# Performance work log

Hardware: AMD Instinct MI355X
Metric: run time of the kernel (lower is better)

## Reference

```python
import jax, jax.numpy as jnp
import numpy as np

B, T, H, W, C = 2, 8, 64, 64, 192
WIN = (4, 8, 8)
SHIFT = (2, 4, 4)
HEADS = 6
HID = 4 * C
N = WIN[0] * WIN[1] * WIN[2]  # 256 tokens per window
CPB_HID = 512


def window_partition(x, win):
    b, t, h, w, c = x.shape
    x = x.reshape(b, t // win[0], win[0], h // win[1], win[1], w // win[2], win[2], c)
    x = x.transpose(0, 1, 3, 5, 2, 4, 6, 7)
    return x.reshape(-1, win[0] * win[1] * win[2], c)


def window_reverse(wins, win, b, t, h, w):
    x = wins.reshape(b, t // win[0], h // win[1], w // win[2], win[0], win[1], win[2], -1)
    x = x.transpose(0, 1, 4, 2, 5, 3, 6, 7)
    return x.reshape(b, t, h, w, -1)


def _rel_coords_table():
    axes = [np.arange(-(WIN[i] - 1), WIN[i], dtype=np.float32) for i in range(3)]
    tbl = np.stack(np.meshgrid(*axes, indexing='ij'), axis=-1)  # (2wt-1,2wh-1,2ww-1,3)
    for i in range(3):
        tbl[..., i] /= WIN[i] - 1
    tbl *= 8.0
    tbl = np.sign(tbl) * np.log2(np.abs(tbl) + 1.0) / np.log2(8.0)
    return tbl.reshape(-1, 3)


def _rel_pos_index():
    coords = np.stack(np.meshgrid(np.arange(WIN[0]), np.arange(WIN[1]), np.arange(WIN[2]), indexing='ij'))
    cf = coords.reshape(3, -1)
    rel = (cf[:, :, None] - cf[:, None, :]).transpose(1, 2, 0)
    rel[..., 0] += WIN[0] - 1
    rel[..., 1] += WIN[1] - 1
    rel[..., 2] += WIN[2] - 1
    rel[..., 0] *= (2 * WIN[1] - 1) * (2 * WIN[2] - 1)
    rel[..., 1] *= 2 * WIN[2] - 1
    return rel.sum(-1)  # (N, N) int


def _attn_mask():
    img = np.zeros((1, T, H, W, 1), dtype=np.float32)
    cnt = 0
    for d in (slice(-WIN[0]), slice(-WIN[0], -SHIFT[0]), slice(-SHIFT[0], None)):
        for h in (slice(-WIN[1]), slice(-WIN[1], -SHIFT[1]), slice(-SHIFT[1], None)):
            for w in (slice(-WIN[2]), slice(-WIN[2], -SHIFT[2]), slice(-SHIFT[2], None)):
                img[:, d, h, w, :] = cnt
                cnt += 1
    mw = window_partition(img, WIN).squeeze(-1)  # (nW, N)
    am = mw[:, None, :] - mw[:, :, None]
    return np.where(am != 0, -100.0, 0.0).astype(np.float32)


REL_TABLE = jnp.asarray(_rel_coords_table())      # (M, 3)
RPI = jnp.asarray(_rel_pos_index().reshape(-1))   # (N*N,)
MASK = jnp.asarray(_attn_mask())                  # (nW, N, N)


def _ln(x, g, b):
    m = x.mean(-1, keepdims=True)
    v = x.var(-1, keepdims=True)
    return (x - m) / jnp.sqrt(v + 1e-5) * g + b


def setup_inputs() -> dict:
    key = jax.random.key(0)
    ks = jax.random.split(key, 16)
    s = lambda fan: 1.0 / np.sqrt(fan)
    return {
        'x': jax.random.normal(ks[0], (B, T, H, W, C), jnp.float32),
        'qkv_w': jax.random.normal(ks[1], (3 * C, C), jnp.float32) * s(C),
        'qkv_b': jnp.zeros((3 * C,), jnp.float32),
        'proj_w': jax.random.normal(ks[2], (C, C), jnp.float32) * s(C),
        'proj_b': jnp.zeros((C,), jnp.float32),
        'cpb_w1': jax.random.normal(ks[3], (CPB_HID, 3), jnp.float32) * s(3),
        'cpb_b1': jnp.zeros((CPB_HID,), jnp.float32),
        'cpb_w2': jax.random.normal(ks[4], (HEADS, CPB_HID), jnp.float32) * s(CPB_HID),
        'logit_scale': jnp.log(10.0 * jnp.ones((HEADS, 1, 1), jnp.float32)),
        'norm1_g': jnp.ones((C,), jnp.float32),
        'norm1_b': jnp.zeros((C,), jnp.float32),
        'norm2_g': jnp.ones((C,), jnp.float32),
        'norm2_b': jnp.zeros((C,), jnp.float32),
        'fc1_w': jax.random.normal(ks[5], (HID, C), jnp.float32) * s(C),
        'fc1_b': jnp.zeros((HID,), jnp.float32),
        'fc2_w': jax.random.normal(ks[6], (C, HID), jnp.float32) * s(HID),
        'fc2_b': jnp.zeros((C,), jnp.float32),
    }


def reference(x, qkv_w, qkv_b, proj_w, proj_b, cpb_w1, cpb_b1, cpb_w2,
              logit_scale, norm1_g, norm1_b, norm2_g, norm2_b,
              fc1_w, fc1_b, fc2_w, fc2_b):
    shortcut = x
    # cyclic shift
    xs = jnp.roll(x, shift=(-SHIFT[0], -SHIFT[1], -SHIFT[2]), axis=(1, 2, 3))
    xw = window_partition(xs, WIN)  # (B*nW, N, C)
    B_ = xw.shape[0]
    d = C // HEADS
    qkv = (xw @ qkv_w.T + qkv_b).reshape(B_, N, 3, HEADS, d).transpose(2, 0, 3, 1, 4)
    q, k, v = qkv[0], qkv[1], qkv[2]  # (B_, h, N, d)
    # cosine attention (F.normalize eps=1e-12)
    qn = q / jnp.maximum(jnp.linalg.norm(q, axis=-1, keepdims=True), 1e-12)
    kn = k / jnp.maximum(jnp.linalg.norm(k, axis=-1, keepdims=True), 1e-12)
    attn = jnp.einsum('bhnd,bhmd->bhnm', qn, kn)
    scale = jnp.exp(jnp.minimum(logit_scale, jnp.log(100.0)))  # clamp at log(1/0.01)
    attn = attn * scale
    # continuous relative position bias
    tbl = jax.nn.relu(REL_TABLE @ cpb_w1.T + cpb_b1) @ cpb_w2.T  # (M, heads)
    bias = tbl[RPI].reshape(N, N, HEADS).transpose(2, 0, 1)      # (h, N, N)
    attn = attn + 16.0 * jax.nn.sigmoid(bias)[None]
    # shift mask
    nW = MASK.shape[0]
    attn = attn.reshape(B_ // nW, nW, HEADS, N, N) + MASK[None, :, None]
    attn = jax.nn.softmax(attn.reshape(B_, HEADS, N, N), axis=-1)
    out = jnp.einsum('bhnm,bhmd->bhnd', attn, v)
    out = out.transpose(0, 2, 1, 3).reshape(B_, N, C)
    out = out @ proj_w.T + proj_b
    xr = window_reverse(out, WIN, B, T, H, W)
    xr = jnp.roll(xr, shift=SHIFT, axis=(1, 2, 3))
    # SwinV2 res-post-norm residual
    x = shortcut + _ln(xr, norm1_g, norm1_b)
    h1 = jax.nn.gelu(x @ fc1_w.T + fc1_b, approximate=False)
    x = x + _ln(h1 @ fc2_w.T + fc2_b, norm2_g, norm2_b)
    return x
```

## Files before the change

### kernel.cpp

```cpp
#include <hip/hip_runtime.h>
#include <math.h>


typedef short short8 __attribute__((ext_vector_type(8)));
typedef short short4v __attribute__((ext_vector_type(4)));
typedef float f32x4 __attribute__((ext_vector_type(4)));

__device__ __forceinline__ short f2bf(float f) {
    union { float f; unsigned u; } v; v.f = f;
    unsigned r = v.u + 0x7FFF + ((v.u >> 16) & 1);
    return (short)(r >> 16);
}

__device__ __forceinline__ float gelu_fast(float x) {
    float s = x * x;
    float t = fmaf(0.044715f, s, 1.0f);
    float y = -1.5957691216057308f * x * t;
    return x * __builtin_amdgcn_rcpf(1.0f + __expf(y));
}

__global__ __launch_bounds__(64) void pack_w_k(const float* __restrict__ w,
                                               short* __restrict__ dst, int K) {
    int lane = threadIdx.x;
    int ktn = K >> 5;
    int nt = blockIdx.x / ktn, kt = blockIdx.x % ktn;
    int r = lane & 15, q = lane >> 4;
    const float* src = w + (size_t)(nt * 16 + r) * K + kt * 32 + q * 8;
    short8 v;
#pragma unroll
    for (int j = 0; j < 8; j++) v[j] = f2bf(src[j]);
    ((short8*)dst)[(size_t)blockIdx.x * 64 + lane] = v;
}

__global__ __launch_bounds__(64) void cpb_table_k(const float* __restrict__ w1,
                                                  const float* __restrict__ b1,
                                                  const float* __restrict__ w2,
                                                  float* __restrict__ tbl6) {
    int m = blockIdx.x;
    int lane = threadIdx.x;
    int it = m / 225;
    int ih = (m / 15) % 15;
    int iw = m % 15;
    float r0 = (float)(it - 3) * (8.0f / 3.0f);
    float r1 = (float)(ih - 7) * (8.0f / 7.0f);
    float r2 = (float)(iw - 7) * (8.0f / 7.0f);
    float c0 = (r0 < 0.f ? -1.f : 1.f) * log2f(fabsf(r0) + 1.0f) * (1.0f / 3.0f);
    float c1 = (r1 < 0.f ? -1.f : 1.f) * log2f(fabsf(r1) + 1.0f) * (1.0f / 3.0f);
    float c2 = (r2 < 0.f ? -1.f : 1.f) * log2f(fabsf(r2) + 1.0f) * (1.0f / 3.0f);
    float hv[8];
#pragma unroll
    for (int j = 0; j < 8; j++) {
        int t = lane * 8 + j;
        hv[j] = fmaxf(0.0f, c0 * w1[3 * t] + c1 * w1[3 * t + 1] + c2 * w1[3 * t + 2] + b1[t]);
    }
#pragma unroll
    for (int head = 0; head < 6; head++) {
        float s = 0.f;
#pragma unroll
        for (int j = 0; j < 8; j++) s += hv[j] * w2[head * 512 + lane * 8 + j];
        s += __shfl_xor(s, 1);
        s += __shfl_xor(s, 2);
        s += __shfl_xor(s, 4);
        s += __shfl_xor(s, 8);
        s += __shfl_xor(s, 16);
        s += __shfl_xor(s, 32);
        if (lane == 0) tbl6[m * 6 + head] = s;
    }
}

__global__ __launch_bounds__(256) void bias_k(const float* __restrict__ tbl6,
                                              float* __restrict__ biasT) {
    int idx = blockIdx.x * 256 + threadIdx.x;
    int h = idx >> 16;
    int rem = idx & 65535;
    int jj = rem >> 8, ii = rem & 255;
    int dt = (ii >> 6) - (jj >> 6) + 3;
    int dh = ((ii >> 3) & 7) - ((jj >> 3) & 7) + 7;
    int dw = (ii & 7) - (jj & 7) + 7;
    int rel = dt * 225 + dh * 15 + dw;
    float v = tbl6[rel * 6 + h];
    biasT[idx] = 16.0f / (1.0f + expf(-v));
}

#define ZSTR 388
__global__ __launch_bounds__(256) void qkv_mfma_k(const float* __restrict__ x,
                                                  const short* __restrict__ wqp,
                                                  const float* __restrict__ qkv_b,
                                                  short* __restrict__ qbf,
                                                  short* __restrict__ kbf,
                                                  short* __restrict__ vtb) {
    __shared__ float Z[32 * ZSTR];
    int tid = threadIdx.x, lane = tid & 63, w = tid >> 6;
    int r = lane & 15, q = lane >> 4;
    int b_ = blockIdx.x >> 3, n0 = (blockIdx.x & 7) << 5;
    int b = b_ >> 7, win = b_ & 127;
    int wt = win >> 6, wh = (win >> 3) & 7, ww = win & 7;

    short8 af[2][6];
#pragma unroll
    for (int m = 0; m < 2; m++) {
        int n = n0 + m * 16 + r;
        int t0 = ((wt * 4 + (n >> 6)) + 2) & 7;
        int h0 = ((wh * 8 + ((n >> 3) & 7)) + 4) & 63;
        int w0 = ((ww * 8 + (n & 7)) + 4) & 63;
        const float* src = x + ((size_t)((b * 8 + t0) * 64 + h0) * 64 + w0) * 192 + q * 8;
#pragma unroll
        for (int kt = 0; kt < 6; kt++) {
            float4 x0 = *(const float4*)(src + kt * 32);
            float4 x1 = *(const float4*)(src + kt * 32 + 4);
            short8 v;
            v[0] = f2bf(x0.x); v[1] = f2bf(x0.y); v[2] = f2bf(x0.z); v[3] = f2bf(x0.w);
            v[4] = f2bf(x1.x); v[5] = f2bf(x1.y); v[6] = f2bf(x1.z); v[7] = f2bf(x1.w);
            af[m][kt] = v;
        }
    }

    for (int ntl = 0; ntl < 9; ntl++) {
        int nt = w * 9 + ntl;
        float bias = qkv_b[nt * 16 + r];
        short8 bfr[6];
#pragma unroll
        for (int kt = 0; kt < 6; kt++)
            bfr[kt] = ((const short8*)wqp)[(size_t)(nt * 6 + kt) * 64 + lane];
        f32x4 a0 = {bias, bias, bias, bias};
        f32x4 a1 = {bias, bias, bias, bias};
#pragma unroll
        for (int kt = 0; kt < 6; kt++) {
            a0 = __builtin_amdgcn_mfma_f32_16x16x32_bf16(af[0][kt], bfr[kt], a0, 0, 0, 0);
            a1 = __builtin_amdgcn_mfma_f32_16x16x32_bf16(af[1][kt], bfr[kt], a1, 0, 0, 0);
        }
        int col = nt * 16 + r;
        if (nt < 24) {
#pragma unroll
            for (int reg = 0; reg < 4; reg++) {
                Z[(q * 4 + reg) * ZSTR + col] = a0[reg];
                Z[(16 + q * 4 + reg) * ZSTR + col] = a1[reg];
            }
        } else {
            int ch = col - 384;
            int hh = ch >> 5, dd = ch & 31;
            short* vb = vtb + ((size_t)(b_ * 6 + hh) * 32 + dd) * 256 + n0;
            short4v p0, p1;
#pragma unroll
            for (int reg = 0; reg < 4; reg++) { p0[reg] = f2bf(a0[reg]); p1[reg] = f2bf(a1[reg]); }
            *(short4v*)(vb + q * 4) = p0;
            *(short4v*)(vb + 16 + q * 4) = p1;
        }
    }
    __syncthreads();
    for (int rw = tid; rw < 384; rw += 256) {
        int token = rw / 12, rr = rw - token * 12;
        int isq = rr < 6 ? 1 : 0;
        int h = isq ? rr : rr - 6;
        const float* rp = &Z[token * ZSTR + rr * 32];
        float ss = 0.f;
#pragma unroll
        for (int d4 = 0; d4 < 8; d4++) {
            f32x4 v4 = *(const f32x4*)(rp + d4 * 4);
            ss += v4[0] * v4[0] + v4[1] * v4[1] + v4[2] * v4[2] + v4[3] * v4[3];
        }
        float inv = 1.0f / fmaxf(sqrtf(ss), 1e-12f);
        short* dst = (isq ? qbf : kbf) + ((size_t)(b_ * 6 + h) * 256 + n0 + token) * 32;
#pragma unroll
        for (int d8 = 0; d8 < 4; d8++) {
            f32x4 a4 = *(const f32x4*)(rp + d8 * 8);
            f32x4 b4 = *(const f32x4*)(rp + d8 * 8 + 4);
            short8 v;
            v[0] = f2bf(a4[0] * inv); v[1] = f2bf(a4[1] * inv);
            v[2] = f2bf(a4[2] * inv); v[3] = f2bf(a4[3] * inv);
            v[4] = f2bf(b4[0] * inv); v[5] = f2bf(b4[1] * inv);
            v[6] = f2bf(b4[2] * inv); v[7] = f2bf(b4[3] * inv);
            *(short8*)(dst + d8 * 8) = v;
        }
    }
}

#define KSTR 40
#define VSTR 264
#define PSTR 40
__global__ __launch_bounds__(256) void attn_mfma_k(const short* __restrict__ qbf,
                                                   const short* __restrict__ kbf,
                                                   const short* __restrict__ vtb,
                                                   const float* __restrict__ biasT,
                                                   const float* __restrict__ logit_scale,
                                                   short* __restrict__ att) {
    __shared__ short Ks[256 * KSTR];
    __shared__ short Vs[32 * VSTR];
    __shared__ short Ps[4][16 * PSTR];
    int tid = threadIdx.x, lane = tid & 63, w = tid >> 6;
    int r = lane & 15, q = lane >> 4;
    int b_ = blockIdx.x / 6, h = blockIdx.x % 6;
    size_t base = (size_t)(b_ * 6 + h) * 8192;

    const short8* kg = (const short8*)(kbf + base);
    const short8* vg = (const short8*)(vtb + base);
    for (int i = tid; i < 1024; i += 256) {
        short8 kv = kg[i];
        *(short8*)&Ks[(i >> 2) * KSTR + (i & 3) * 8] = kv;
        short8 vv = vg[i];
        *(short8*)&Vs[(i >> 5) * VSTR + (i & 31) * 8] = vv;
    }

    short8 qf[4];
#pragma unroll
    for (int mt = 0; mt < 4; mt++)
        qf[mt] = *(const short8*)(qbf + base + (size_t)(w * 64 + mt * 16 + r) * 32 + q * 8);

    float scale = __expf(fminf(logit_scale[h], 4.6051702f));
    float M = scale + 16.0f;
    int win = b_ & 127;
    int wt4 = (win >> 6) * 4, wh8 = ((win >> 3) & 7) * 8, ww8 = (win & 7) * 8;
    auto region = [&](int n) {
        int ts = wt4 + (n >> 6), hs = wh8 + ((n >> 3) & 7), wsv = ww8 + (n & 7);
        int rt = ts < 4 ? 0 : (ts < 6 ? 1 : 2);
        int rh = hs < 56 ? 0 : (hs < 60 ? 1 : 2);
        int rw = wsv < 56 ? 0 : (wsv < 60 ? 1 : 2);
        return rt * 9 + rh * 3 + rw;
    };
    int rowreg[4][4];
#pragma unroll
    for (int mt = 0; mt < 4; mt++)
#pragma unroll
        for (int reg = 0; reg < 4; reg++)
            rowreg[mt][reg] = region(w * 64 + mt * 16 + q * 4 + reg);

    f32x4 O[4][2];
    float lp[4][4];
#pragma unroll
    for (int mt = 0; mt < 4; mt++) {
        O[mt][0] = (f32x4){0.f, 0.f, 0.f, 0.f};
        O[mt][1] = (f32x4){0.f, 0.f, 0.f, 0.f};
#pragma unroll
        for (int reg = 0; reg < 4; reg++) lp[mt][reg] = 0.f;
    }
    __syncthreads();

    const float* bh = biasT + ((size_t)h << 16);
    for (int s = 0; s < 8; s++) {
        short8 kf0 = *(const short8*)&Ks[(s * 32 + r) * KSTR + q * 8];
        short8 kf1 = *(const short8*)&Ks[(s * 32 + 16 + r) * KSTR + q * 8];
        short8 vf0 = *(const short8*)&Vs[r * VSTR + s * 32 + q * 8];
        short8 vf1 = *(const short8*)&Vs[(16 + r) * VSTR + s * 32 + q * 8];
        int cr0 = region(s * 32 + r);
        int cr1 = region(s * 32 + 16 + r);
#pragma unroll
        for (int mt = 0; mt < 4; mt++) {
            f32x4 s0 = {0.f, 0.f, 0.f, 0.f};
            f32x4 s1 = {0.f, 0.f, 0.f, 0.f};
            s0 = __builtin_amdgcn_mfma_f32_16x16x32_bf16(qf[mt], kf0, s0, 0, 0, 0);
            s1 = __builtin_amdgcn_mfma_f32_16x16x32_bf16(qf[mt], kf1, s1, 0, 0, 0);
            int qcol = w * 64 + mt * 16 + q * 4;
            float4 b0 = *(const float4*)(bh + (size_t)(s * 32 + r) * 256 + qcol);
            float4 b1 = *(const float4*)(bh + (size_t)(s * 32 + 16 + r) * 256 + qcol);
#pragma unroll
            for (int reg = 0; reg < 4; reg++) {
                float bb0 = (reg == 0 ? b0.x : reg == 1 ? b0.y : reg == 2 ? b0.z : b0.w);
                float bb1 = (reg == 0 ? b1.x : reg == 1 ? b1.y : reg == 2 ? b1.z : b1.w);
                float v0 = s0[reg] * scale + bb0 + (cr0 == rowreg[mt][reg] ? 0.f : -100.f) - M;
                float v1 = s1[reg] * scale + bb1 + (cr1 == rowreg[mt][reg] ? 0.f : -100.f) - M;
                float p0 = __expf(v0);
                float p1 = __expf(v1);
                lp[mt][reg] += p0 + p1;
                Ps[w][(q * 4 + reg) * PSTR + r] = f2bf(p0);
                Ps[w][(q * 4 + reg) * PSTR + 16 + r] = f2bf(p1);
            }
            short8 pa = *(const short8*)&Ps[w][r * PSTR + q * 8];
            O[mt][0] = __builtin_amdgcn_mfma_f32_16x16x32_bf16(vf0, pa, O[mt][0], 0, 0, 0);
            O[mt][1] = __builtin_amdgcn_mfma_f32_16x16x32_bf16(vf1, pa, O[mt][1], 0, 0, 0);
        }
    }

#pragma unroll
    for (int mt = 0; mt < 4; mt++)
#pragma unroll
        for (int reg = 0; reg < 4; reg++) {
            float v = lp[mt][reg];
            v += __shfl_xor(v, 1);
            v += __shfl_xor(v, 2);
            v += __shfl_xor(v, 4);
            v += __shfl_xor(v, 8);
            lp[mt][reg] = 1.0f / v;
        }
#pragma unroll
    for (int mt = 0; mt < 4; mt++) {
        int srcl = (r >> 2) << 4;
        float t0 = __shfl(lp[mt][0], srcl);
        float t1 = __shfl(lp[mt][1], srcl);
        float t2 = __shfl(lp[mt][2], srcl);
        float t3 = __shfl(lp[mt][3], srcl);
        int rm = r & 3;
        float linv = rm == 0 ? t0 : (rm == 1 ? t1 : (rm == 2 ? t2 : t3));
        int query = w * 64 + mt * 16 + r;
        short* dst = att + ((size_t)b_ * 256 + query) * 192 + h * 32 + q * 4;
#pragma unroll
        for (int nt = 0; nt < 2; nt++) {
            short4v pv;
#pragma unroll
            for (int reg = 0; reg < 4; reg++) pv[reg] = f2bf(O[mt][nt][reg] * linv);
            *(short4v*)(dst + nt * 16) = pv;
        }
    }
}

__global__ __launch_bounds__(256) void proj_mfma_k(const short* __restrict__ att,
                                                   const short* __restrict__ wpp,
                                                   const float* __restrict__ proj_b,
                                                   const float* __restrict__ x,
                                                   const float* __restrict__ g1,
                                                   const float* __restrict__ b1n,
                                                   float* __restrict__ out,
                                                   short* __restrict__ xmb) {
    __shared__ float Z[32 * 196];
    __shared__ float ps[32][8];
    __shared__ float pss[32][8];
    __shared__ float mean_s[32], inv_s[32];
    int tid = threadIdx.x, lane = tid & 63, w = tid >> 6;
    int r = lane & 15, q = lane >> 4;
    int b_ = blockIdx.x >> 3, n0 = (blockIdx.x & 7) << 5;

    short8 af[2][6];
#pragma unroll
    for (int m = 0; m < 2; m++) {
        const short* src = att + ((size_t)b_ * 256 + n0 + m * 16 + r) * 192 + q * 8;
#pragma unroll
        for (int kt = 0; kt < 6; kt++)
            af[m][kt] = *(const short8*)(src + kt * 32);
    }
    for (int ntl = 0; ntl < 3; ntl++) {
        int nt = w * 3 + ntl;
        f32x4 binit = *(const f32x4*)(proj_b + nt * 16 + q * 4);
        short8 bfr[6];
#pragma unroll
        for (int kt = 0; kt < 6; kt++)
            bfr[kt] = ((const short8*)wpp)[(size_t)(nt * 6 + kt) * 64 + lane];
        f32x4 a0 = binit, a1 = binit;
#pragma unroll
        for (int kt = 0; kt < 6; kt++) {
            a0 = __builtin_amdgcn_mfma_f32_16x16x32_bf16(bfr[kt], af[0][kt], a0, 0, 0, 0);
            a1 = __builtin_amdgcn_mfma_f32_16x16x32_bf16(bfr[kt], af[1][kt], a1, 0, 0, 0);
        }
        *(f32x4*)&Z[(r) * 196 + nt * 16 + q * 4] = a0;
        *(f32x4*)&Z[(16 + r) * 196 + nt * 16 + q * 4] = a1;
    }
    __syncthreads();
    {
        int token = tid >> 3, part = tid & 7;
        float s = 0.f, ss = 0.f;
        const float* zr = &Z[token * 196 + part * 24];
#pragma unroll
        for (int c = 0; c < 24; c++) { float v = zr[c]; s += v; ss += v * v; }
        ps[token][part] = s; pss[token][part] = ss;
    }
    __syncthreads();
    if (tid < 32) {
        float s = 0.f, ss = 0.f;
#pragma unroll
        for (int p = 0; p < 8; p++) { s += ps[tid][p]; ss += pss[tid][p]; }
        float mean = s * (1.0f / 192.0f);
        float var = ss * (1.0f / 192.0f) - mean * mean;
        mean_s[tid] = mean;
        inv_s[tid] = 1.0f / sqrtf(var + 1e-5f);
    }
    __syncthreads();
    int b = b_ >> 7, win = b_ & 127;
    int wt = win >> 6, wh = (win >> 3) & 7, ww = win & 7;
#pragma unroll
    for (int k = 0; k < 6; k++) {
        int idx = k * 256 + tid;
        int token = idx / 48;
        int c4 = (idx - token * 48) * 4;
        int n = n0 + token;
        int t0 = ((wt * 4 + (n >> 6)) + 2) & 7;
        int h0 = ((wh * 8 + ((n >> 3) & 7)) + 4) & 63;
        int w0 = ((ww * 8 + (n & 7)) + 4) & 63;
        size_t gb = ((size_t)((b * 8 + t0) * 64 + h0) * 64 + w0) * 192 + c4;
        float mean = mean_s[token], inv = inv_s[token];
        f32x4 zv = *(const f32x4*)&Z[token * 196 + c4];
        f32x4 gv = *(const f32x4*)(g1 + c4);
        f32x4 bv = *(const f32x4*)(b1n + c4);
        f32x4 xv = *(const f32x4*)(x + gb);
        f32x4 o;
        short4v xm;
#pragma unroll
        for (int j = 0; j < 4; j++) {
            o[j] = xv[j] + (zv[j] - mean) * inv * gv[j] + bv[j];
            xm[j] = f2bf(o[j]);
        }
        *(f32x4*)(out + gb) = o;
        *(short4v*)(xmb + gb) = xm;
    }
}

#define XSTR 200
#define H2STR 264
__global__ __launch_bounds__(512, 4) void mlp_mfma_k(const short* __restrict__ xmb,
                                                     const short* __restrict__ w1p,
                                                     const short* __restrict__ w2p,
                                                     const float* __restrict__ fc1_b,
                                                     const float* __restrict__ fc2_b,
                                                     const float* __restrict__ g2,
                                                     const float* __restrict__ b2,
                                                     float* __restrict__ out) {
    __shared__ short Xs[64 * XSTR];
    __shared__ short Hs[64 * H2STR];
    __shared__ float ps[64][4], pss[64][4];
    __shared__ float mean_s[64], inv_s[64];
    int tid = threadIdx.x;
    int lane = tid & 63, w = tid >> 6;
    int r = lane & 15, q = lane >> 4;
    size_t tok0 = (size_t)blockIdx.x * 64;

    for (int i = tid; i < 1536; i += 512) {
        int token = i / 24, ch8 = (i - token * 24) * 8;
        short8 v = *(const short8*)(xmb + (tok0 + token) * 192 + ch8);
        *(short8*)&Xs[token * XSTR + ch8] = v;
    }
    __syncthreads();

    int mg = w >> 2;
    int ng = w & 3;
    f32x4 acc2[6];
#pragma unroll
    for (int i = 0; i < 6; i++) acc2[i] = (f32x4){0.f, 0.f, 0.f, 0.f};

    for (int c = 0; c < 3; c++) {
        {
            int ntg0 = c * 16 + 2 * w;
            f32x4 a[2][4];
#pragma unroll
            for (int ntl = 0; ntl < 2; ntl++) {
                f32x4 binit = *(const f32x4*)(fc1_b + (ntg0 + ntl) * 16 + q * 4);
#pragma unroll
                for (int m = 0; m < 4; m++) a[ntl][m] = binit;
            }
#pragma unroll
            for (int kt = 0; kt < 6; kt++) {
                short8 w0 = ((const short8*)w1p)[(size_t)((ntg0) * 6 + kt) * 64 + lane];
                short8 w1f = ((const short8*)w1p)[(size_t)((ntg0 + 1) * 6 + kt) * 64 + lane];
                short8 xb[4];
#pragma unroll
                for (int m = 0; m < 4; m++)
                    xb[m] = *(const short8*)&Xs[(m * 16 + r) * XSTR + kt * 32 + q * 8];
#pragma unroll
                for (int m = 0; m < 4; m++) {
                    a[0][m] = __builtin_amdgcn_mfma_f32_16x16x32_bf16(w0, xb[m], a[0][m], 0, 0, 0);
                    a[1][m] = __builtin_amdgcn_mfma_f32_16x16x32_bf16(w1f, xb[m], a[1][m], 0, 0, 0);
                }
            }
#pragma unroll
            for (int ntl = 0; ntl < 2; ntl++) {
                int hcol = (2 * w + ntl) * 16 + q * 4;
#pragma unroll
                for (int m = 0; m < 4; m++) {
                    short4v p;
#pragma unroll
                    for (int reg = 0; reg < 4; reg++) p[reg] = f2bf(gelu_fast(a[ntl][m][reg]));
                    *(short4v*)&Hs[(m * 16 + r) * H2STR + hcol] = p;
                }
            }
        }
        __syncthreads();

#pragma unroll
        for (int kk = 0; kk < 8; kk++) {
            short8 hb0 = *(const short8*)&Hs[((mg * 2) * 16 + r) * H2STR + kk * 32 + q * 8];
            short8 hb1 = *(const short8*)&Hs[((mg * 2 + 1) * 16 + r) * H2STR + kk * 32 + q * 8];
            int kkg = c * 8 + kk;
#pragma unroll
            for (int n = 0; n < 3; n++) {
                int ntz = ng * 3 + n;
                short8 wf = ((const short8*)w2p)[(size_t)(ntz * 24 + kkg) * 64 + lane];
                acc2[n * 2 + 0] = __builtin_amdgcn_mfma_f32_16x16x32_bf16(wf, hb0, acc2[n * 2 + 0], 0, 0, 0);
                acc2[n * 2 + 1] = __builtin_amdgcn_mfma_f32_16x16x32_bf16(wf, hb1, acc2[n * 2 + 1], 0, 0, 0);
            }
        }
        __syncthreads();
    }

    float s0 = 0.f, ss0 = 0.f, s1 = 0.f, ss1 = 0.f;
#pragma unroll
    for (int n = 0; n < 3; n++) {
        f32x4 b4 = *(const f32x4*)(fc2_b + (ng * 3 + n) * 16 + q * 4);
        f32x4 z0 = acc2[n * 2 + 0] + b4;
        f32x4 z1 = acc2[n * 2 + 1] + b4;
        acc2[n * 2 + 0] = z0;
        acc2[n * 2 + 1] = z1;
#pragma unroll
        for (int reg = 0; reg < 4; reg++) {
            s0 += z0[reg]; ss0 += z0[reg] * z0[reg];
            s1 += z1[reg]; ss1 += z1[reg] * z1[reg];
        }
    }
    s0 += __shfl_xor(s0, 16); ss0 += __shfl_xor(ss0, 16);
    s0 += __shfl_xor(s0, 32); ss0 += __shfl_xor(ss0, 32);
    s1 += __shfl_xor(s1, 16); ss1 += __shfl_xor(ss1, 16);
    s1 += __shfl_xor(s1, 32); ss1 += __shfl_xor(ss1, 32);
    if (q == 0) {
        int t0 = mg * 32 + r;
        ps[t0][ng] = s0;  pss[t0][ng] = ss0;
        ps[t0 + 16][ng] = s1;  pss[t0 + 16][ng] = ss1;
    }
    __syncthreads();
    if (tid < 64) {
        float sm = ps[tid][0] + ps[tid][1] + ps[tid][2] + ps[tid][3];
        float sq = pss[tid][0] + pss[tid][1] + pss[tid][2] + pss[tid][3];
        float mean = sm * (1.0f / 192.0f);
        float var = sq * (1.0f / 192.0f) - mean * mean;
        mean_s[tid] = mean;
        inv_s[tid] = 1.0f / sqrtf(var + 1e-5f);
    }
    __syncthreads();
#pragma unroll
    for (int n = 0; n < 3; n++) {
        int ntz = ng * 3 + n;
        f32x4 g4 = *(const f32x4*)(g2 + ntz * 16 + q * 4);
        f32x4 bb4 = *(const f32x4*)(b2 + ntz * 16 + q * 4);
#pragma unroll
        for (int mh = 0; mh < 2; mh++) {
            int token = mg * 32 + mh * 16 + r;
            float mean = mean_s[token], inv = inv_s[token];
            size_t gi = (tok0 + token) * 192 + ntz * 16 + q * 4;
            f32x4 o = *(const f32x4*)(out + gi);
            f32x4 z = acc2[n * 2 + mh];
            f32x4 res;
#pragma unroll
            for (int reg = 0; reg < 4; reg++)
                res[reg] = o[reg] + (z[reg] - mean) * inv * g4[reg] + bb4[reg];
            *(f32x4*)(out + gi) = res;
        }
    }
}

extern "C" void kernel_launch(void* const* d_in, const int* in_sizes, int n_in,
                              void* d_out, int out_size, void* d_ws, size_t ws_size,
                              hipStream_t stream) {
    const float* x           = (const float*)d_in[0];
    const float* qkv_w       = (const float*)d_in[1];
    const float* qkv_b       = (const float*)d_in[2];
    const float* proj_w      = (const float*)d_in[3];
    const float* proj_b      = (const float*)d_in[4];
    const float* cpb_w1      = (const float*)d_in[5];
    const float* cpb_b1      = (const float*)d_in[6];
    const float* cpb_w2      = (const float*)d_in[7];
    const float* logit_scale = (const float*)d_in[8];
    const float* norm1_g     = (const float*)d_in[9];
    const float* norm1_b     = (const float*)d_in[10];
    const float* norm2_g     = (const float*)d_in[11];
    const float* norm2_b     = (const float*)d_in[12];
    const float* fc1_w       = (const float*)d_in[13];
    const float* fc1_b       = (const float*)d_in[14];
    const float* fc2_w       = (const float*)d_in[15];
    const float* fc2_b       = (const float*)d_in[16];
    float* out = (float*)d_out;

    float* ws = (float*)d_ws;
    const size_t QKVE = (size_t)256 * 6 * 256 * 32;
    short* att    = (short*)ws;
    float* biasT  = ws + QKVE;
    float* tbl6   = biasT + (size_t)6 * 256 * 256;
    short* w1pack = (short*)(tbl6 + 9472);
    short* w2pack = w1pack + (size_t)768 * 192;
    short* wqpack = w2pack + (size_t)192 * 768;
    short* wppack = wqpack + (size_t)576 * 192;
    short* qbf    = wppack + (size_t)192 * 192;
    short* kbf    = qbf + QKVE;
    short* vtb    = kbf + QKVE;
    short* xmb    = vtb + QKVE;

    hipLaunchKernelGGL(pack_w_k, dim3(288), dim3(64), 0, stream, fc1_w, w1pack, 192);
    hipLaunchKernelGGL(pack_w_k, dim3(288), dim3(64), 0, stream, fc2_w, w2pack, 768);
    hipLaunchKernelGGL(pack_w_k, dim3(216), dim3(64), 0, stream, qkv_w, wqpack, 192);
    hipLaunchKernelGGL(pack_w_k, dim3(72), dim3(64), 0, stream, proj_w, wppack, 192);
    hipLaunchKernelGGL(cpb_table_k, dim3(1575), dim3(64), 0, stream, cpb_w1, cpb_b1, cpb_w2, tbl6);
    hipLaunchKernelGGL(bias_k, dim3(1536), dim3(256), 0, stream, tbl6, biasT);
    hipLaunchKernelGGL(qkv_mfma_k, dim3(2048), dim3(256), 0, stream, x, wqpack, qkv_b, qbf, kbf, vtb);
    hipLaunchKernelGGL(attn_mfma_k, dim3(1536), dim3(256), 0, stream, qbf, kbf, vtb, biasT, logit_scale, att);
    hipLaunchKernelGGL(proj_mfma_k, dim3(2048), dim3(256), 0, stream, att, wppack, proj_b, x, norm1_g, norm1_b, out, xmb);
    hipLaunchKernelGGL(mlp_mfma_k, dim3(1024), dim3(512), 0, stream, xmb, w1pack, w2pack,
                       fc1_b, fc2_b, norm2_g, norm2_b, out);
}
```

Baseline: 366.6 us.

## Pack attention bias as fp16 interleaved; keep proj LN in registers; pad MLP LDS

The relative-position bias table is now stored as fp16 in a layout that interleaves the two key halves, so each attention lane reads its bias with one 16-byte load instead of two float4 loads. This halves the bias traffic in the attention inner loop at the cost of fp16 rounding of the bias. The projection kernel no longer stages results in a large LDS buffer: layer-norm statistics are reduced with shuffles directly from the MFMA accumulators, and the residual output is written from registers, which removes shared-memory traffic and some synchronisation. The MLP LDS row strides are also padded slightly, likely to avoid bank conflicts.

After: 367.7 us. No clear change (+0.3%).

```diff
diff --git a/kernel.cpp b/kernel.cpp
--- a/kernel.cpp
+++ b/kernel.cpp
@@ -10,6 +10,13 @@
     union { float f; unsigned u; } v; v.f = f;
     unsigned r = v.u + 0x7FFF + ((v.u >> 16) & 1);
     return (short)(r >> 16);
+}
+__device__ __forceinline__ short f2h(float f) {
+    _Float16 h = (_Float16)f;
+    union { _Float16 h; short s; } u; u.h = h; return u.s;
+}
+__device__ __forceinline__ float h2f(short s) {
+    union { _Float16 h; short s; } u; u.s = s; return (float)u.h;
 }
 
 __device__ __forceinline__ float gelu_fast(float x) {
@@ -69,17 +76,20 @@
 }
 
 __global__ __launch_bounds__(256) void bias_k(const float* __restrict__ tbl6,
-                                              float* __restrict__ biasT) {
+                                              short* __restrict__ biasPK) {
     int idx = blockIdx.x * 256 + threadIdx.x;
+    int kh = idx & 1;
+    int query = (idx >> 1) & 255;
+    int r = (idx >> 9) & 15;
+    int s = (idx >> 13) & 7;
     int h = idx >> 16;
-    int rem = idx & 65535;
-    int jj = rem >> 8, ii = rem & 255;
-    int dt = (ii >> 6) - (jj >> 6) + 3;
-    int dh = ((ii >> 3) & 7) - ((jj >> 3) & 7) + 7;
-    int dw = (ii & 7) - (jj & 7) + 7;
+    int key = s * 32 + kh * 16 + r;
+    int dt = (query >> 6) - (key >> 6) + 3;
+    int dh = ((query >> 3) & 7) - ((key >> 3) & 7) + 7;
+    int dw = (query & 7) - (key & 7) + 7;
     int rel = dt * 225 + dh * 15 + dw;
     float v = tbl6[rel * 6 + h];
-    biasT[idx] = 16.0f / (1.0f + expf(-v));
+    biasPK[idx] = f2h(16.0f / (1.0f + expf(-v)));
 }
 
 #define ZSTR 388
@@ -181,7 +191,7 @@
 __global__ __launch_bounds__(256) void attn_mfma_k(const short* __restrict__ qbf,
                                                    const short* __restrict__ kbf,
                                                    const short* __restrict__ vtb,
-                                                   const float* __restrict__ biasT,
+                                                   const short* __restrict__ biasPK,
                                                    const float* __restrict__ logit_scale,
                                                    short* __restrict__ att) {
     __shared__ short Ks[256 * KSTR];
@@ -235,7 +245,7 @@
     }
     __syncthreads();
 
-    const float* bh = biasT + ((size_t)h << 16);
+    const short* bh = biasPK + ((size_t)h << 16);
     for (int s = 0; s < 8; s++) {
         short8 kf0 = *(const short8*)&Ks[(s * 32 + r) * KSTR + q * 8];
         short8 kf1 = *(const short8*)&Ks[(s * 32 + 16 + r) * KSTR + q * 8];
@@ -250,12 +260,11 @@
             s0 = __builtin_amdgcn_mfma_f32_16x16x32_bf16(qf[mt], kf0, s0, 0, 0, 0);
             s1 = __builtin_amdgcn_mfma_f32_16x16x32_bf16(qf[mt], kf1, s1, 0, 0, 0);
             int qcol = w * 64 + mt * 16 + q * 4;
-            float4 b0 = *(const float4*)(bh + (size_t)(s * 32 + r) * 256 + qcol);
-            float4 b1 = *(const float4*)(bh + (size_t)(s * 32 + 16 + r) * 256 + qcol);
+            short8 bv = *(const short8*)(bh + (size_t)(s * 16 + r) * 512 + qcol * 2);
 #pragma unroll
             for (int reg = 0; reg < 4; reg++) {
-                float bb0 = (reg == 0 ? b0.x : reg == 1 ? b0.y : reg == 2 ? b0.z : b0.w);
-                float bb1 = (reg == 0 ? b1.x : reg == 1 ? b1.y : reg == 2 ? b1.z : b1.w);
+                float bb0 = h2f(bv[2 * reg]);
+                float bb1 = h2f(bv[2 * reg + 1]);
                 float v0 = s0[reg] * scale + bb0 + (cr0 == rowreg[mt][reg] ? 0.f : -100.f) - M;
                 float v1 = s1[reg] * scale + bb1 + (cr1 == rowreg[mt][reg] ? 0.f : -100.f) - M;
                 float p0 = __expf(v0);
@@ -310,9 +319,7 @@
                                                    const float* __restrict__ b1n,
                                                    float* __restrict__ out,
                                                    short* __restrict__ xmb) {
-    __shared__ float Z[32 * 196];
-    __shared__ float ps[32][8];
-    __shared__ float pss[32][8];
+    __shared__ float ps[32][4], pss[32][4];
     __shared__ float mean_s[32], inv_s[32];
     int tid = threadIdx.x, lane = tid & 63, w = tid >> 6;
     int r = lane & 15, q = lane >> 4;
@@ -326,6 +333,8 @@
         for (int kt = 0; kt < 6; kt++)
             af[m][kt] = *(const short8*)(src + kt * 32);
     }
+    f32x4 acc[3][2];
+#pragma unroll
     for (int ntl = 0; ntl < 3; ntl++) {
         int nt = w * 3 + ntl;
         f32x4 binit = *(const f32x4*)(proj_b + nt * 16 + q * 4);
@@ -339,25 +348,32 @@
             a0 = __builtin_amdgcn_mfma_f32_16x16x32_bf16(bfr[kt], af[0][kt], a0, 0, 0, 0);
             a1 = __builtin_amdgcn_mfma_f32_16x16x32_bf16(bfr[kt], af[1][kt], a1, 0, 0, 0);
         }
-        *(f32x4*)&Z[(r) * 196 + nt * 16 + q * 4] = a0;
-        *(f32x4*)&Z[(16 + r) * 196 + nt * 16 + q * 4] = a1;
-    }
-    __syncthreads();
-    {
-        int token = tid >> 3, part = tid & 7;
-        float s = 0.f, ss = 0.f;
-        const float* zr = &Z[token * 196 + part * 24];
-#pragma unroll
-        for (int c = 0; c < 24; c++) { float v = zr[c]; s += v; ss += v * v; }
-        ps[token][part] = s; pss[token][part] = ss;
+        acc[ntl][0] = a0;
+        acc[ntl][1] = a1;
+    }
+    float s0 = 0.f, ss0 = 0.f, s1 = 0.f, ss1 = 0.f;
+#pragma unroll
+    for (int ntl = 0; ntl < 3; ntl++)
+#pragma unroll
+        for (int reg = 0; reg < 4; reg++) {
+            float z0 = acc[ntl][0][reg], z1 = acc[ntl][1][reg];
+            s0 += z0; ss0 += z0 * z0;
+            s1 += z1; ss1 += z1 * z1;
+        }
+    s0 += __shfl_xor(s0, 16); ss0 += __shfl_xor(ss0, 16);
+    s0 += __shfl_xor(s0, 32); ss0 += __shfl_xor(ss0, 32);
+    s1 += __shfl_xor(s1, 16); ss1 += __shfl_xor(ss1, 16);
+    s1 += __shfl_xor(s1, 32); ss1 += __shfl_xor(ss1, 32);
+    if (q == 0) {
+        ps[r][w] = s0;  pss[r][w] = ss0;
+        ps[16 + r][w] = s1;  pss[16 + r][w] = ss1;
     }
     __syncthreads();
     if (tid < 32) {
-        float s = 0.f, ss = 0.f;
-#pragma unroll
-        for (int p = 0; p < 8; p++) { s += ps[tid][p]; ss += pss[tid][p]; }
-        float mean = s * (1.0f / 192.0f);
-        float var = ss * (1.0f / 192.0f) - mean * mean;
+        float sm = ps[tid][0] + ps[tid][1] + ps[tid][2] + ps[tid][3];
+        float sq = pss[tid][0] + pss[tid][1] + pss[tid][2] + pss[tid][3];
+        float mean = sm * (1.0f / 192.0f);
+        float var = sq * (1.0f / 192.0f) - mean * mean;
         mean_s[tid] = mean;
         inv_s[tid] = 1.0f / sqrtf(var + 1e-5f);
     }
@@ -365,34 +381,36 @@
     int b = b_ >> 7, win = b_ & 127;
     int wt = win >> 6, wh = (win >> 3) & 7, ww = win & 7;
 #pragma unroll
-    for (int k = 0; k < 6; k++) {
-        int idx = k * 256 + tid;
-        int token = idx / 48;
-        int c4 = (idx - token * 48) * 4;
+    for (int mh = 0; mh < 2; mh++) {
+        int token = mh * 16 + r;
         int n = n0 + token;
         int t0 = ((wt * 4 + (n >> 6)) + 2) & 7;
         int h0 = ((wh * 8 + ((n >> 3) & 7)) + 4) & 63;
         int w0 = ((ww * 8 + (n & 7)) + 4) & 63;
-        size_t gb = ((size_t)((b * 8 + t0) * 64 + h0) * 64 + w0) * 192 + c4;
+        size_t gb = ((size_t)((b * 8 + t0) * 64 + h0) * 64 + w0) * 192;
         float mean = mean_s[token], inv = inv_s[token];
-        f32x4 zv = *(const f32x4*)&Z[token * 196 + c4];
-        f32x4 gv = *(const f32x4*)(g1 + c4);
-        f32x4 bv = *(const f32x4*)(b1n + c4);
-        f32x4 xv = *(const f32x4*)(x + gb);
-        f32x4 o;
-        short4v xm;
-#pragma unroll
-        for (int j = 0; j < 4; j++) {
-            o[j] = xv[j] + (zv[j] - mean) * inv * gv[j] + bv[j];
-            xm[j] = f2bf(o[j]);
-        }
-        *(f32x4*)(out + gb) = o;
-        *(short4v*)(xmb + gb) = xm;
-    }
-}
-
-#define XSTR 200
-#define H2STR 264
+#pragma unroll
+        for (int ntl = 0; ntl < 3; ntl++) {
+            int ch = (w * 3 + ntl) * 16 + q * 4;
+            f32x4 zv = acc[ntl][mh];
+            f32x4 gv = *(const f32x4*)(g1 + ch);
+            f32x4 bv = *(const f32x4*)(b1n + ch);
+            f32x4 xv = *(const f32x4*)(x + gb + ch);
+            f32x4 o;
+            short4v xm;
+#pragma unroll
+            for (int j = 0; j < 4; j++) {
+                o[j] = xv[j] + (zv[j] - mean) * inv * gv[j] + bv[j];
+                xm[j] = f2bf(o[j]);
+            }
+            *(f32x4*)(out + gb + ch) = o;
+            *(short4v*)(xmb + gb + ch) = xm;
+        }
+    }
+}
+
+#define XSTR 204
+#define H2STR 268
 __global__ __launch_bounds__(512, 4) void mlp_mfma_k(const short* __restrict__ xmb,
                                                      const short* __restrict__ w1p,
                                                      const short* __restrict__ w2p,
@@ -556,8 +574,8 @@
     float* ws = (float*)d_ws;
     const size_t QKVE = (size_t)256 * 6 * 256 * 32;
     short* att    = (short*)ws;
-    float* biasT  = ws + QKVE;
-    float* tbl6   = biasT + (size_t)6 * 256 * 256;
+    short* biasPK = (short*)(ws + QKVE);
+    float* tbl6   = ws + QKVE + (size_t)6 * 256 * 256;
     short* w1pack = (short*)(tbl6 + 9472);
     short* w2pack = w1pack + (size_t)768 * 192;
     short* wqpack = w2pack + (size_t)192 * 768;
@@ -572,9 +590,9 @@
     hipLaunchKernelGGL(pack_w_k, dim3(216), dim3(64), 0, stream, qkv_w, wqpack, 192);
     hipLaunchKernelGGL(pack_w_k, dim3(72), dim3(64), 0, stream, proj_w, wppack, 192);
     hipLaunchKernelGGL(cpb_table_k, dim3(1575), dim3(64), 0, stream, cpb_w1, cpb_b1, cpb_w2, tbl6);
-    hipLaunchKernelGGL(bias_k, dim3(1536), dim3(256), 0, stream, tbl6, biasT);
+    hipLaunchKernelGGL(bias_k, dim3(1536), dim3(256), 0, stream, tbl6, biasPK);
     hipLaunchKernelGGL(qkv_mfma_k, dim3(2048), dim3(256), 0, stream, x, wqpack, qkv_b, qbf, kbf, vtb);
-    hipLaunchKernelGGL(attn_mfma_k, dim3(1536), dim3(256), 0, stream, qbf, kbf, vtb, biasT, logit_scale, att);
+    hipLaunchKernelGGL(attn_mfma_k, dim3(1536), dim3(256), 0, stream, qbf, kbf, vtb, biasPK, logit_scale, att);
     hipLaunchKernelGGL(proj_mfma_k, dim3(2048), dim3(256), 0, stream, att, wppack, proj_b, x, norm1_g, norm1_b, out, xmb);
     hipLaunchKernelGGL(mlp_mfma_k, dim3(1024), dim3(512), 0, stream, xmb, w1pack, w2pack,
                        fc1_b, fc2_b, norm2_g, norm2_b, out);
```
